# Kernel tuning notes

Hardware: AMD Instinct MI355X
Metric: run time of the kernel (lower is better)

## Reference

```python
import jax, jax.numpy as jnp
import numpy as np

B, M, FIN, K, FOUT, NNZ = 8, 40000, 64, 6, 64, 320000

def setup_inputs() -> dict:
    key = jax.random.key(0)
    k1, k2, k3, k4, k5 = jax.random.split(key, 5)
    x = jax.random.normal(k1, (B, M, FIN), dtype=jnp.float32)
    edge_rows = jax.random.randint(k2, (NNZ,), 0, M)
    edge_cols = jax.random.randint(k3, (NNZ,), 0, M)
    edge_vals = jax.random.normal(k4, (NNZ,), dtype=jnp.float32) * 0.1
    W = jax.random.normal(k5, (FIN * K, FOUT), dtype=jnp.float32) * 0.05
    return {"x": x, "edge_vals": edge_vals, "W": W,
            "edge_rows": edge_rows, "edge_cols": edge_cols}

def reference(x, edge_vals, W, edge_rows, edge_cols):
    Bd, Md, Fin = x.shape
    nK = W.shape[0] // Fin
    Fout = W.shape[1]
    # x0: [M, Fin*B] as in tf.transpose([1,2,0]) + reshape
    x0 = jnp.transpose(x, (1, 2, 0)).reshape(Md, Fin * Bd)

    def spmm_rescaled(v):
        # rescale_L(L, lmax=2) = L - I, so (L - I) @ v = L@v - v
        Lv = jax.ops.segment_sum(edge_vals[:, None] * v[edge_cols],
                                 edge_rows, num_segments=Md)
        return Lv - v

    xs = [x0]
    if nK > 1:
        x1 = spmm_rescaled(x0)
        xs.append(x1)
        xp, xc = x0, x1
        for _ in range(2, nK):
            xn = 2.0 * spmm_rescaled(xc) - xp  # Chebyshev recurrence
            xs.append(xn)
            xp, xc = xc, xn
    X = jnp.stack(xs, axis=0)                     # [K, M, Fin*B]
    X = X.reshape(nK, Md, Fin, Bd)                # split Fin*B -> (Fin, B)
    X = jnp.transpose(X, (3, 1, 2, 0))            # [B, M, Fin, K]
    X = X.reshape(Bd * Md, Fin * nK)
    out = (X @ W).reshape(Bd, Md, Fout)           # dense projection
    return out
```

## Files before the change

### kernel.cpp

```cpp
#include <hip/hip_runtime.h>

#define Mn    40000
#define Bn    8
#define FINn  64
#define Kn    6
#define FOUTn 64
#define NNZn  320000
#define Cn    512
#define NB    ((Mn + 255) / 256)
#define MT    (Mn / 64)


typedef _Float16 half8 __attribute__((ext_vector_type(8)));
typedef __attribute__((ext_vector_type(4))) float floatx4;

__device__ __forceinline__ ushort f2h(float f) {
    _Float16 h = (_Float16)f;
    return *(ushort*)&h;
}


__global__ __launch_bounds__(256) void k_hist(const int* __restrict__ rows,
                                              int* __restrict__ cnt) {
    int e = blockIdx.x * 256 + threadIdx.x;
    if (e < NNZn) atomicAdd(&cnt[rows[e]], 1);
}

__global__ __launch_bounds__(256) void k_scan_part(const int* __restrict__ cnt,
                                                   int* __restrict__ rowptr,
                                                   int* __restrict__ bsum) {
    __shared__ int part[256];
    int tid = threadIdx.x;
    int r = blockIdx.x * 256 + tid;
    int v = (r < Mn) ? cnt[r] : 0;
    part[tid] = v;
    __syncthreads();
    for (int off = 1; off < 256; off <<= 1) {
        int t = (tid >= off) ? part[tid - off] : 0;
        __syncthreads();
        part[tid] += t;
        __syncthreads();
    }
    if (r < Mn) rowptr[r] = part[tid] - v;
    if (tid == 255) bsum[blockIdx.x] = part[255];
}

__global__ __launch_bounds__(256) void k_scan_bsums(const int* __restrict__ bsum,
                                                    int* __restrict__ boff,
                                                    int* __restrict__ rowptr) {
    __shared__ int part[256];
    int tid = threadIdx.x;
    int v = (tid < NB) ? bsum[tid] : 0;
    part[tid] = v;
    __syncthreads();
    for (int off = 1; off < 256; off <<= 1) {
        int t = (tid >= off) ? part[tid - off] : 0;
        __syncthreads();
        part[tid] += t;
        __syncthreads();
    }
    if (tid < NB) boff[tid] = part[tid] - v;
    if (tid == 255) rowptr[Mn] = part[255];
}

__global__ __launch_bounds__(256) void k_scan_add(int* __restrict__ rowptr,
                                                  const int* __restrict__ boff,
                                                  int* __restrict__ wcur) {
    int r = blockIdx.x * 256 + threadIdx.x;
    if (r < Mn) {
        int v = rowptr[r] + boff[blockIdx.x];
        rowptr[r] = v;
        wcur[r] = v;
    }
}

__global__ __launch_bounds__(256) void k_scatter(const int* __restrict__ rows,
                                                 const int* __restrict__ cols,
                                                 const float* __restrict__ vals,
                                                 int* __restrict__ wcur,
                                                 int2* __restrict__ csr) {
    int e = blockIdx.x * 256 + threadIdx.x;
    if (e < NNZn) {
        int p = atomicAdd(&wcur[rows[e]], 1);
        int2 cv; cv.x = cols[e]; cv.y = __float_as_int(vals[e]);
        csr[p] = cv;
    }
}


__global__ __launch_bounds__(256) void k_transpose_h(const float* __restrict__ x,
                                                     ushort* __restrict__ x0h) {
    int m0 = blockIdx.x * 4;
    int t  = threadIdx.x;
#pragma unroll
    for (int k = 0; k < 2; ++k) {
        int i   = t + k * 256;
        int ml  = i >> 7;
        int rem = i & 127;
        int b   = rem >> 4;
        int fq  = (rem & 15) * 4;
        float4 a = *(const float4*)(x + ((size_t)b * Mn + m0 + ml) * 64 + fq);
        union { uint2 u; ushort h[4]; } s;
        s.h[0] = f2h(a.x); s.h[1] = f2h(a.y); s.h[2] = f2h(a.z); s.h[3] = f2h(a.w);
        *(uint2*)(x0h + (size_t)(m0 + ml) * Cn + b * 64 + fq) = s.u;
    }
}


__device__ __forceinline__ void fmah8(float* a, uint4 g, float w) {
    union { uint4 u; _Float16 h[8]; } c; c.u = g;
#pragma unroll
    for (int i = 0; i < 8; ++i) a[i] += w * (float)c.h[i];
}

__global__ __launch_bounds__(256) void k_spmm_h(const ushort* __restrict__ xc,
                                                const ushort* __restrict__ xp,
                                                ushort* __restrict__ xn,
                                                const int* __restrict__ rowptr,
                                                const int2* __restrict__ csr,
                                                int first) {
    int t = threadIdx.x;
    int lane = t & 63;
    int m = blockIdx.x * 4 + (t >> 6);
    const uint4* xc4 = (const uint4*)xc;
    uint4 v = xc4[(size_t)m * 64 + lane];
    uint4 p;
    if (!first) p = ((const uint4*)xp)[(size_t)m * 64 + lane];
    float a[8];
    { union { uint4 u; _Float16 h[8]; } c; c.u = v;
#pragma unroll
      for (int i = 0; i < 8; ++i) a[i] = -(float)c.h[i]; }

    int e = rowptr[m], end = rowptr[m + 1];
    for (; e + 8 <= end; e += 8) {
        int2 cv[8];
#pragma unroll
        for (int i = 0; i < 8; ++i) cv[i] = csr[e + i];
        uint4 g[8];
#pragma unroll
        for (int i = 0; i < 8; ++i) g[i] = xc4[(size_t)cv[i].x * 64 + lane];
#pragma unroll
        for (int i = 0; i < 8; ++i) fmah8(a, g[i], __int_as_float(cv[i].y));
    }
    for (; e + 4 <= end; e += 4) {
        int2 cv0 = csr[e],     cv1 = csr[e + 1];
        int2 cv2 = csr[e + 2], cv3 = csr[e + 3];
        uint4 g0 = xc4[(size_t)cv0.x * 64 + lane];
        uint4 g1 = xc4[(size_t)cv1.x * 64 + lane];
        uint4 g2 = xc4[(size_t)cv2.x * 64 + lane];
        uint4 g3 = xc4[(size_t)cv3.x * 64 + lane];
        fmah8(a, g0, __int_as_float(cv0.y));
        fmah8(a, g1, __int_as_float(cv1.y));
        fmah8(a, g2, __int_as_float(cv2.y));
        fmah8(a, g3, __int_as_float(cv3.y));
    }
    for (; e < end; ++e) {
        int2 cv = csr[e];
        uint4 g = xc4[(size_t)cv.x * 64 + lane];
        fmah8(a, g, __int_as_float(cv.y));
    }

    if (!first) {
        union { uint4 u; _Float16 h[8]; } c; c.u = p;
#pragma unroll
        for (int i = 0; i < 8; ++i) a[i] = 2.f * a[i] - (float)c.h[i];
    }
    union { uint4 u; _Float16 h[8]; } s;
#pragma unroll
    for (int i = 0; i < 8; ++i) s.h[i] = (_Float16)a[i];
    ((uint4*)xn)[(size_t)m * 64 + lane] = s.u;
}


__global__ __launch_bounds__(256) void k_wfrag(const float* __restrict__ W,
                                               ushort* __restrict__ wfrag) {
    int idx = blockIdx.x * 256 + threadIdx.x;
    if (idx >= 12 * 4 * 64 * 8) return;
    int j    = idx & 7;
    int lane = (idx >> 3) & 63;
    int n    = (idx >> 9) & 3;
    int kk   = idx >> 11;
    int k    = (lane >> 4) * 8 + j;
    int lev  = kk >> 1;
    int f    = (kk & 1) * 32 + k;
    int fo   = n * 16 + (lane & 15);
    wfrag[idx] = f2h(W[(f * Kn + lev) * FOUTn + fo]);
}


__global__ __launch_bounds__(256, 2) void k_gemm_mfma(const ushort* __restrict__ xh,
                                                      const ushort* __restrict__ wfrag,
                                                      float* __restrict__ out) {
    int t     = threadIdx.x;
    int wv    = t >> 6;
    int lane  = t & 63;
    int q     = lane >> 4, r = lane & 15;
    int mtile = blockIdx.x % MT;
    int b     = blockIdx.x / MT;
    int m0    = mtile * 64;

    const size_t lstrideH = (size_t)Mn * Cn;
    const ushort* abase = xh + (size_t)(m0 + wv * 16 + r) * Cn + b * 64 + q * 8;

    half8 aA0 = *(const half8*)(abase);
    half8 aB0 = *(const half8*)(abase + 32);
    half8 aA1 = *(const half8*)(abase + 1 * lstrideH);
    half8 aB1 = *(const half8*)(abase + 1 * lstrideH + 32);
    half8 aA2 = *(const half8*)(abase + 2 * lstrideH);
    half8 aB2 = *(const half8*)(abase + 2 * lstrideH + 32);
    half8 aA3 = *(const half8*)(abase + 3 * lstrideH);
    half8 aB3 = *(const half8*)(abase + 3 * lstrideH + 32);
    half8 aA4 = *(const half8*)(abase + 4 * lstrideH);
    half8 aB4 = *(const half8*)(abase + 4 * lstrideH + 32);
    half8 aA5 = *(const half8*)(abase + 5 * lstrideH);
    half8 aB5 = *(const half8*)(abase + 5 * lstrideH + 32);
    __builtin_amdgcn_sched_barrier(0);

    floatx4 acc[4];
    acc[0] = (floatx4)0.f; acc[1] = (floatx4)0.f;
    acc[2] = (floatx4)0.f; acc[3] = (floatx4)0.f;

#define MC_HALF(kkg, af)                                                              \
    do {                                                                              \
        const ushort* wf = wfrag + ((size_t)((kkg) * 4) * 64 + lane) * 8;             \
        acc[0] = __builtin_amdgcn_mfma_f32_16x16x32_f16(af, *(const half8*)(wf),        acc[0], 0, 0, 0); \
        acc[1] = __builtin_amdgcn_mfma_f32_16x16x32_f16(af, *(const half8*)(wf + 512),  acc[1], 0, 0, 0); \
        acc[2] = __builtin_amdgcn_mfma_f32_16x16x32_f16(af, *(const half8*)(wf + 1024), acc[2], 0, 0, 0); \
        acc[3] = __builtin_amdgcn_mfma_f32_16x16x32_f16(af, *(const half8*)(wf + 1536), acc[3], 0, 0, 0); \
    } while (0)

    MC_HALF(0,  aA0); MC_HALF(1,  aB0);
    MC_HALF(2,  aA1); MC_HALF(3,  aB1);
    MC_HALF(4,  aA2); MC_HALF(5,  aB2);
    MC_HALF(6,  aA3); MC_HALF(7,  aB3);
    MC_HALF(8,  aA4); MC_HALF(9,  aB4);
    MC_HALF(10, aA5); MC_HALF(11, aB5);
#undef MC_HALF

    size_t obase = ((size_t)b * Mn + m0 + wv * 16) * FOUTn;
#pragma unroll
    for (int n = 0; n < 4; ++n) {
#pragma unroll
        for (int reg = 0; reg < 4; ++reg) {
            int orow = q * 4 + reg;
            out[obase + (size_t)orow * FOUTn + n * 16 + r] = acc[n][reg];
        }
    }
}


__global__ __launch_bounds__(512) void k_transpose_f(const float* __restrict__ x,
                                                     float* __restrict__ x0) {
    int m = blockIdx.x, t = threadIdx.x;
    int b = t >> 6, f = t & 63;
    x0[(size_t)m * Cn + t] = x[((size_t)b * Mn + m) * 64 + f];
}

__global__ __launch_bounds__(256) void k_spmm_f32(const float4* __restrict__ xc,
                                                  const float4* __restrict__ xp,
                                                  float4* __restrict__ xn,
                                                  const int* __restrict__ rowptr,
                                                  const int2* __restrict__ csr,
                                                  int first) {
    int t = threadIdx.x;
    int lane = t & 63;
    int m = blockIdx.x * 4 + (t >> 6);
    size_t rb = (size_t)m * 128;
    float4 v0 = xc[rb + lane];
    float4 v1 = xc[rb + 64 + lane];
    float4 a0 = make_float4(-v0.x, -v0.y, -v0.z, -v0.w);
    float4 a1 = make_float4(-v1.x, -v1.y, -v1.z, -v1.w);
    int e = rowptr[m], end = rowptr[m + 1];
    for (; e < end; ++e) {
        int2 cv = csr[e];
        float w = __int_as_float(cv.y);
        const float4* r = xc + (size_t)cv.x * 128;
        float4 g0 = r[lane], g1 = r[64 + lane];
        a0.x += w * g0.x; a0.y += w * g0.y; a0.z += w * g0.z; a0.w += w * g0.w;
        a1.x += w * g1.x; a1.y += w * g1.y; a1.z += w * g1.z; a1.w += w * g1.w;
    }
    if (!first) {
        float4 p0 = xp[rb + lane];
        float4 p1 = xp[rb + 64 + lane];
        a0.x = 2.f * a0.x - p0.x; a0.y = 2.f * a0.y - p0.y;
        a0.z = 2.f * a0.z - p0.z; a0.w = 2.f * a0.w - p0.w;
        a1.x = 2.f * a1.x - p1.x; a1.y = 2.f * a1.y - p1.y;
        a1.z = 2.f * a1.z - p1.z; a1.w = 2.f * a1.w - p1.w;
    }
    xn[rb + lane] = a0;
    xn[rb + 64 + lane] = a1;
}

__global__ __launch_bounds__(256) void k_gemm2(const float* __restrict__ xa,
                                               const float* __restrict__ xb,
                                               const float* __restrict__ W,
                                               float* __restrict__ out,
                                               int ka, int kb, int accum) {
    __shared__ __align__(16) float Wa[64 * 64];
    __shared__ __align__(16) float Wb[64 * 64];
    __shared__ __align__(16) float xsa[4 * Cn];
    __shared__ __align__(16) float xsb[4 * Cn];
    int t = threadIdx.x;
    size_t m0 = (size_t)blockIdx.x * 4;
    for (int i = t; i < 4096; i += 256) {
        int f = i >> 6, fo = i & 63;
        Wa[i] = W[(f * Kn + ka) * FOUTn + fo];
        Wb[i] = W[(f * Kn + kb) * FOUTn + fo];
    }
    for (int i = t; i < 4 * Cn; i += 256) {
        xsa[i] = xa[m0 * Cn + i];
        xsb[i] = xb[m0 * Cn + i];
    }
    __syncthreads();
    int fo  = (t & 15) * 4;
    int idx = t >> 4;
    int m   = idx & 3;
    int bq  = idx >> 2;
    float4 acc0 = make_float4(0.f, 0.f, 0.f, 0.f);
    float4 acc1 = make_float4(0.f, 0.f, 0.f, 0.f);
    for (int f = 0; f < 64; ++f) {
        float4 wa = *(const float4*)&Wa[f * 64 + fo];
        float a0 = xsa[m * Cn + bq * 64 + f];
        float a1 = xsa[m * Cn + (bq + 4) * 64 + f];
        acc0.x += a0 * wa.x; acc0.y += a0 * wa.y; acc0.z += a0 * wa.z; acc0.w += a0 * wa.w;
        acc1.x += a1 * wa.x; acc1.y += a1 * wa.y; acc1.z += a1 * wa.z; acc1.w += a1 * wa.w;
        float4 wb = *(const float4*)&Wb[f * 64 + fo];
        float b0 = xsb[m * Cn + bq * 64 + f];
        float b1 = xsb[m * Cn + (bq + 4) * 64 + f];
        acc0.x += b0 * wb.x; acc0.y += b0 * wb.y; acc0.z += b0 * wb.z; acc0.w += b0 * wb.w;
        acc1.x += b1 * wb.x; acc1.y += b1 * wb.y; acc1.z += b1 * wb.z; acc1.w += b1 * wb.w;
    }
    size_t o0 = (((size_t)bq * Mn) + (m0 + m)) * FOUTn + fo;
    size_t o1 = (((size_t)(bq + 4) * Mn) + (m0 + m)) * FOUTn + fo;
    float4* out4_0 = (float4*)&out[o0];
    float4* out4_1 = (float4*)&out[o1];
    if (accum) {
        float4 c0 = *out4_0, c1 = *out4_1;
        acc0.x += c0.x; acc0.y += c0.y; acc0.z += c0.z; acc0.w += c0.w;
        acc1.x += c1.x; acc1.y += c1.y; acc1.z += c1.z; acc1.w += c1.w;
    }
    *out4_0 = acc0;
    *out4_1 = acc1;
}


extern "C" void kernel_launch(void* const* d_in, const int* in_sizes, int n_in,
                              void* d_out, int out_size, void* d_ws, size_t ws_size,
                              hipStream_t stream) {
    const float* x         = (const float*)d_in[0];
    const float* edge_vals = (const float*)d_in[1];
    const float* W         = (const float*)d_in[2];
    const int*   edge_rows = (const int*)d_in[3];
    const int*   edge_cols = (const int*)d_in[4];
    float* out = (float*)d_out;

    char* ws = (char*)d_ws;
    const size_t bufB = (size_t)Mn * Cn * sizeof(float);
    const size_t bufH = (size_t)Mn * Cn * sizeof(ushort);
    const size_t wfB  = 12 * 4 * 64 * 8 * sizeof(ushort);
    const size_t csrB = (size_t)(Mn + 4 + Mn) * 4 + (size_t)NNZn * 8;

    const int spmm_grid = Mn / 4;
    const int gemm_grid = MT * 8;

    if (ws_size >= 6 * bufH + wfB + csrB) {
        ushort* xh  = (ushort*)ws;
        ushort* wfr = (ushort*)(ws + 6 * bufH);
        int*    rowptr = (int*)(ws + 6 * bufH + wfB);
        int*    fill   = rowptr + (Mn + 4);
        int2*   csr    = (int2*)(fill + Mn);
        int*    bsum   = (int*)csr;
        int*    boff   = bsum + 256;
        ushort* slot[6];
        for (int l = 0; l < 6; ++l) slot[l] = xh + (size_t)l * Mn * Cn;

        hipMemsetAsync(fill, 0, Mn * sizeof(int), stream);
        k_hist<<<(NNZn + 255) / 256, 256, 0, stream>>>(edge_rows, fill);
        k_scan_part<<<NB, 256, 0, stream>>>(fill, rowptr, bsum);
        k_scan_bsums<<<1, 256, 0, stream>>>(bsum, boff, rowptr);
        k_scan_add<<<NB, 256, 0, stream>>>(rowptr, boff, fill);
        k_scatter<<<(NNZn + 255) / 256, 256, 0, stream>>>(edge_rows, edge_cols,
                                                          edge_vals, fill, csr);
        k_wfrag<<<96, 256, 0, stream>>>(W, wfr);

        k_transpose_h<<<Mn / 4, 256, 0, stream>>>(x, slot[0]);
        k_spmm_h<<<spmm_grid, 256, 0, stream>>>(slot[0], slot[0], slot[1],
                                                rowptr, csr, 1);
        k_spmm_h<<<spmm_grid, 256, 0, stream>>>(slot[1], slot[0], slot[2],
                                                rowptr, csr, 0);
        k_spmm_h<<<spmm_grid, 256, 0, stream>>>(slot[2], slot[1], slot[3],
                                                rowptr, csr, 0);
        k_spmm_h<<<spmm_grid, 256, 0, stream>>>(slot[3], slot[2], slot[4],
                                                rowptr, csr, 0);
        k_spmm_h<<<spmm_grid, 256, 0, stream>>>(slot[4], slot[3], slot[5],
                                                rowptr, csr, 0);
        k_gemm_mfma<<<gemm_grid, 256, 0, stream>>>(xh, wfr, out);
    } else {
        float* buf0 = (float*)(ws);
        float* buf1 = (float*)(ws + bufB);
        float* buf2 = (float*)(ws + 2 * bufB);
        int*   rowptr = (int*)(ws + 3 * bufB);
        int*   fill   = rowptr + (Mn + 4);
        int2*  csr    = (int2*)(fill + Mn);
        int*   bsum   = (int*)csr;
        int*   boff   = bsum + 256;
        hipMemsetAsync(fill, 0, Mn * sizeof(int), stream);
        k_hist<<<(NNZn + 255) / 256, 256, 0, stream>>>(edge_rows, fill);
        k_scan_part<<<NB, 256, 0, stream>>>(fill, rowptr, bsum);
        k_scan_bsums<<<1, 256, 0, stream>>>(bsum, boff, rowptr);
        k_scan_add<<<NB, 256, 0, stream>>>(rowptr, boff, fill);
        k_scatter<<<(NNZn + 255) / 256, 256, 0, stream>>>(edge_rows, edge_cols,
                                                          edge_vals, fill, csr);
        k_transpose_f<<<Mn, 512, 0, stream>>>(x, buf0);
        k_spmm_f32<<<spmm_grid, 256, 0, stream>>>((const float4*)buf0, (const float4*)buf0,
                                                  (float4*)buf1, rowptr, csr, 1);
        k_gemm2<<<Mn / 4, 256, 0, stream>>>(buf0, buf1, W, out, 0, 1, 0);
        k_spmm_f32<<<spmm_grid, 256, 0, stream>>>((const float4*)buf1, (const float4*)buf0,
                                                  (float4*)buf2, rowptr, csr, 0);
        k_spmm_f32<<<spmm_grid, 256, 0, stream>>>((const float4*)buf2, (const float4*)buf1,
                                                  (float4*)buf0, rowptr, csr, 0);
        k_gemm2<<<Mn / 4, 256, 0, stream>>>(buf2, buf0, W, out, 2, 3, 1);
        k_spmm_f32<<<spmm_grid, 256, 0, stream>>>((const float4*)buf0, (const float4*)buf2,
                                                  (float4*)buf1, rowptr, csr, 0);
        k_spmm_f32<<<spmm_grid, 256, 0, stream>>>((const float4*)buf1, (const float4*)buf0,
                                                  (float4*)buf2, rowptr, csr, 0);
        k_gemm2<<<Mn / 4, 256, 0, stream>>>(buf1, buf2, W, out, 4, 5, 1);
    }
}
```

Before: 543.8 us.

## Column-block SpMM grid for cache locality and LDS-staged A tiles in MFMA GEMM

The half-precision SpMM now splits the 512 feature columns into 8 blocks of 64 and launches a separate grid slice per block. Each wave covers 8 rows by 8 lanes, so gathered neighbour rows touch a narrower column slice that is more likely to stay in cache. The edge loop becomes a wave-uniform loop over the longest row's degree with masked padding, which adds wasted iterations on uneven rows. The GEMM loads its A tiles into swizzled LDS via global_load_lds before the MFMAs, where before it used direct register loads; this adds LDS traffic and a barrier. The fp32 fallback path is left unchanged apart from its launch sizes.

New measurement: 552.6 us. About the same (+1.6%).

```diff
diff --git a/kernel.cpp b/kernel.cpp
--- a/kernel.cpp
+++ b/kernel.cpp
@@ -9,6 +9,8 @@
 #define Cn    512
 #define NB    ((Mn + 255) / 256)
 #define MT    (Mn / 64)
+#define NCB   8
+#define MCH   (Mn / 32)
 
 
 typedef _Float16 half8 __attribute__((ext_vector_type(8)));
@@ -17,6 +19,12 @@
 __device__ __forceinline__ ushort f2h(float f) {
     _Float16 h = (_Float16)f;
     return *(ushort*)&h;
+}
+
+__device__ __forceinline__ void gl_lds16(const ushort* g, ushort* l) {
+    __builtin_amdgcn_global_load_lds(
+        (const __attribute__((address_space(1))) unsigned int*)g,
+        (__attribute__((address_space(3))) unsigned int*)l, 16, 0, 0);
 }
 
 
@@ -119,45 +127,38 @@
                                                 const int* __restrict__ rowptr,
                                                 const int2* __restrict__ csr,
                                                 int first) {
-    int t = threadIdx.x;
+    int t    = threadIdx.x;
     int lane = t & 63;
-    int m = blockIdx.x * 4 + (t >> 6);
+    int wv   = t >> 6;
+    int cblk = blockIdx.x / MCH;
+    int mch  = blockIdx.x % MCH;
+    int r    = mch * 32 + wv * 8 + (lane >> 3);
+    int coff = cblk * 8 + (lane & 7);
+
     const uint4* xc4 = (const uint4*)xc;
-    uint4 v = xc4[(size_t)m * 64 + lane];
+    uint4 v = xc4[(size_t)r * 64 + coff];
     uint4 p;
-    if (!first) p = ((const uint4*)xp)[(size_t)m * 64 + lane];
+    if (!first) p = ((const uint4*)xp)[(size_t)r * 64 + coff];
+    int rp0 = rowptr[r], rp1 = rowptr[r + 1];
+
     float a[8];
     { union { uint4 u; _Float16 h[8]; } c; c.u = v;
 #pragma unroll
       for (int i = 0; i < 8; ++i) a[i] = -(float)c.h[i]; }
 
-    int e = rowptr[m], end = rowptr[m + 1];
-    for (; e + 8 <= end; e += 8) {
-        int2 cv[8];
-#pragma unroll
-        for (int i = 0; i < 8; ++i) cv[i] = csr[e + i];
-        uint4 g[8];
-#pragma unroll
-        for (int i = 0; i < 8; ++i) g[i] = xc4[(size_t)cv[i].x * 64 + lane];
-#pragma unroll
-        for (int i = 0; i < 8; ++i) fmah8(a, g[i], __int_as_float(cv[i].y));
-    }
-    for (; e + 4 <= end; e += 4) {
-        int2 cv0 = csr[e],     cv1 = csr[e + 1];
-        int2 cv2 = csr[e + 2], cv3 = csr[e + 3];
-        uint4 g0 = xc4[(size_t)cv0.x * 64 + lane];
-        uint4 g1 = xc4[(size_t)cv1.x * 64 + lane];
-        uint4 g2 = xc4[(size_t)cv2.x * 64 + lane];
-        uint4 g3 = xc4[(size_t)cv3.x * 64 + lane];
-        fmah8(a, g0, __int_as_float(cv0.y));
-        fmah8(a, g1, __int_as_float(cv1.y));
-        fmah8(a, g2, __int_as_float(cv2.y));
-        fmah8(a, g3, __int_as_float(cv3.y));
-    }
-    for (; e < end; ++e) {
-        int2 cv = csr[e];
-        uint4 g = xc4[(size_t)cv.x * 64 + lane];
-        fmah8(a, g, __int_as_float(cv.y));
+    int it = 0;
+    while (__any(rp0 + it < rp1)) {
+#pragma unroll
+        for (int u = 0; u < 4; ++u) {
+            int e  = rp0 + it + u;
+            int ec = (e < rp1) ? e : (rp1 - 1);
+            ec = (ec < 0) ? 0 : ec;
+            int2 cv = csr[ec];
+            float w = (e < rp1) ? __int_as_float(cv.y) : 0.f;
+            uint4 g = xc4[(size_t)cv.x * 64 + coff];
+            fmah8(a, g, w);
+        }
+        it += 4;
     }
 
     if (!first) {
@@ -168,7 +169,7 @@
     union { uint4 u; _Float16 h[8]; } s;
 #pragma unroll
     for (int i = 0; i < 8; ++i) s.h[i] = (_Float16)a[i];
-    ((uint4*)xn)[(size_t)m * 64 + lane] = s.u;
+    ((uint4*)xn)[(size_t)r * 64 + coff] = s.u;
 }
 
 
@@ -191,6 +192,7 @@
 __global__ __launch_bounds__(256, 2) void k_gemm_mfma(const ushort* __restrict__ xh,
                                                       const ushort* __restrict__ wfrag,
                                                       float* __restrict__ out) {
+    __shared__ __align__(16) ushort As[6][64 * 64];
     int t     = threadIdx.x;
     int wv    = t >> 6;
     int lane  = t & 63;
@@ -200,41 +202,40 @@
     int m0    = mtile * 64;
 
     const size_t lstrideH = (size_t)Mn * Cn;
-    const ushort* abase = xh + (size_t)(m0 + wv * 16 + r) * Cn + b * 64 + q * 8;
-
-    half8 aA0 = *(const half8*)(abase);
-    half8 aB0 = *(const half8*)(abase + 32);
-    half8 aA1 = *(const half8*)(abase + 1 * lstrideH);
-    half8 aB1 = *(const half8*)(abase + 1 * lstrideH + 32);
-    half8 aA2 = *(const half8*)(abase + 2 * lstrideH);
-    half8 aB2 = *(const half8*)(abase + 2 * lstrideH + 32);
-    half8 aA3 = *(const half8*)(abase + 3 * lstrideH);
-    half8 aB3 = *(const half8*)(abase + 3 * lstrideH + 32);
-    half8 aA4 = *(const half8*)(abase + 4 * lstrideH);
-    half8 aB4 = *(const half8*)(abase + 4 * lstrideH + 32);
-    half8 aA5 = *(const half8*)(abase + 5 * lstrideH);
-    half8 aB5 = *(const half8*)(abase + 5 * lstrideH + 32);
-    __builtin_amdgcn_sched_barrier(0);
+
+    int srow = wv * 8 + (lane >> 3);
+    int gsw  = (lane & 7) ^ (srow & 7);
+    const ushort* gs0 = xh + (size_t)(m0 + srow) * Cn + b * 64 + gsw * 8;
+    const ushort* gs1 = gs0 + (size_t)32 * Cn;
+#pragma unroll
+    for (int lev = 0; lev < 6; ++lev) {
+        gl_lds16(gs0 + lev * lstrideH, &As[lev][wv * 512]);
+        gl_lds16(gs1 + lev * lstrideH, &As[lev][2048 + wv * 512]);
+    }
+    __syncthreads();
 
     floatx4 acc[4];
     acc[0] = (floatx4)0.f; acc[1] = (floatx4)0.f;
     acc[2] = (floatx4)0.f; acc[3] = (floatx4)0.f;
 
-#define MC_HALF(kkg, af)                                                              \
+    int row = wv * 16 + r;
+#define MC_HALF(lev, half)                                                            \
     do {                                                                              \
-        const ushort* wf = wfrag + ((size_t)((kkg) * 4) * 64 + lane) * 8;             \
+        int gran = ((half) * 4 + q) ^ (row & 7);                                      \
+        half8 af = *(const half8*)&As[lev][row * 64 + (gran << 3)];                   \
+        const ushort* wf = wfrag + ((size_t)(((lev) * 2 + (half)) * 4) * 64 + lane) * 8; \
         acc[0] = __builtin_amdgcn_mfma_f32_16x16x32_f16(af, *(const half8*)(wf),        acc[0], 0, 0, 0); \
         acc[1] = __builtin_amdgcn_mfma_f32_16x16x32_f16(af, *(const half8*)(wf + 512),  acc[1], 0, 0, 0); \
         acc[2] = __builtin_amdgcn_mfma_f32_16x16x32_f16(af, *(const half8*)(wf + 1024), acc[2], 0, 0, 0); \
         acc[3] = __builtin_amdgcn_mfma_f32_16x16x32_f16(af, *(const half8*)(wf + 1536), acc[3], 0, 0, 0); \
     } while (0)
 
-    MC_HALF(0,  aA0); MC_HALF(1,  aB0);
-    MC_HALF(2,  aA1); MC_HALF(3,  aB1);
-    MC_HALF(4,  aA2); MC_HALF(5,  aB2);
-    MC_HALF(6,  aA3); MC_HALF(7,  aB3);
-    MC_HALF(8,  aA4); MC_HALF(9,  aB4);
-    MC_HALF(10, aA5); MC_HALF(11, aB5);
+    MC_HALF(0, 0); MC_HALF(0, 1);
+    MC_HALF(1, 0); MC_HALF(1, 1);
+    MC_HALF(2, 0); MC_HALF(2, 1);
+    MC_HALF(3, 0); MC_HALF(3, 1);
+    MC_HALF(4, 0); MC_HALF(4, 1);
+    MC_HALF(5, 0); MC_HALF(5, 1);
 #undef MC_HALF
 
     size_t obase = ((size_t)b * Mn + m0 + wv * 16) * FOUTn;
@@ -360,7 +361,7 @@
     const size_t wfB  = 12 * 4 * 64 * 8 * sizeof(ushort);
     const size_t csrB = (size_t)(Mn + 4 + Mn) * 4 + (size_t)NNZn * 8;
 
-    const int spmm_grid = Mn / 4;
+    const int spmm_grid = NCB * MCH;
     const int gemm_grid = MT * 8;
 
     if (ws_size >= 6 * bufH + wfB + csrB) {
@@ -412,18 +413,18 @@
         k_scatter<<<(NNZn + 255) / 256, 256, 0, stream>>>(edge_rows, edge_cols,
                                                           edge_vals, fill, csr);
         k_transpose_f<<<Mn, 512, 0, stream>>>(x, buf0);
-        k_spmm_f32<<<spmm_grid, 256, 0, stream>>>((const float4*)buf0, (const float4*)buf0,
-                                                  (float4*)buf1, rowptr, csr, 1);
+        k_spmm_f32<<<Mn / 4, 256, 0, stream>>>((const float4*)buf0, (const float4*)buf0,
+                                               (float4*)buf1, rowptr, csr, 1);
         k_gemm2<<<Mn / 4, 256, 0, stream>>>(buf0, buf1, W, out, 0, 1, 0);
-        k_spmm_f32<<<spmm_grid, 256, 0, stream>>>((const float4*)buf1, (const float4*)buf0,
-                                                  (float4*)buf2, rowptr, csr, 0);
-        k_spmm_f32<<<spmm_grid, 256, 0, stream>>>((const float4*)buf2, (const float4*)buf1,
-                                                  (float4*)buf0, rowptr, csr, 0);
+        k_spmm_f32<<<Mn / 4, 256, 0, stream>>>((const float4*)buf1, (const float4*)buf0,
+                                               (float4*)buf2, rowptr, csr, 0);
+        k_spmm_f32<<<Mn / 4, 256, 0, stream>>>((const float4*)buf2, (const float4*)buf1,
+                                               (float4*)buf0, rowptr, csr, 0);
         k_gemm2<<<Mn / 4, 256, 0, stream>>>(buf2, buf0, W, out, 2, 3, 1);
-        k_spmm_f32<<<spmm_grid, 256, 0, stream>>>((const float4*)buf0, (const float4*)buf2,
-                                                  (float4*)buf1, rowptr, csr, 0);
-        k_spmm_f32<<<spmm_grid, 256, 0, stream>>>((const float4*)buf1, (const float4*)buf0,
-                                                  (float4*)buf2, rowptr, csr, 0);
+        k_spmm_f32<<<Mn / 4, 256, 0, stream>>>((const float4*)buf0, (const float4*)buf2,
+                                               (float4*)buf1, rowptr, csr, 0);
+        k_spmm_f32<<<Mn / 4, 256, 0, stream>>>((const float4*)buf1, (const float4*)buf0,
+                                               (float4*)buf2, rowptr, csr, 0);
         k_gemm2<<<Mn / 4, 256, 0, stream>>>(buf1, buf2, W, out, 4, 5, 1);
     }
 }
```

## Stage GEMM A-tiles through LDS with double-buffered async loads

Applied to the files above, without the earlier changes.

The MFMA projection kernel no longer loads all six Chebyshev levels into registers up front. It now streams each level into a double-buffered, XOR-swizzled LDS tile using global_load_lds, with manual vmcnt waits, so loading level k+2 overlaps with the MFMAs for level k. Launch bounds rise to 4 waves per SIMD to allow higher occupancy. The fallback f32 path's spmm grid is also changed to Mn/4, which may be a different block count from before and does not run by default. The manual waitcnt handling relies on exact counts of outstanding loads, so any miscount would read stale LDS data.

Result: no change. 540.4 us (-0.6%).

```diff
diff --git a/kernel.cpp b/kernel.cpp
--- a/kernel.cpp
+++ b/kernel.cpp
@@ -17,6 +17,12 @@
 __device__ __forceinline__ ushort f2h(float f) {
     _Float16 h = (_Float16)f;
     return *(ushort*)&h;
+}
+
+__device__ __forceinline__ void gl_lds16(const ushort* g, ushort* l) {
+    __builtin_amdgcn_global_load_lds(
+        (const __attribute__((address_space(1))) unsigned int*)g,
+        (__attribute__((address_space(3))) unsigned int*)l, 16, 0, 0);
 }
 
 
@@ -188,9 +194,10 @@
 }
 
 
-__global__ __launch_bounds__(256, 2) void k_gemm_mfma(const ushort* __restrict__ xh,
+__global__ __launch_bounds__(256, 4) void k_gemm_mfma(const ushort* __restrict__ xh,
                                                       const ushort* __restrict__ wfrag,
                                                       float* __restrict__ out) {
+    __shared__ __align__(16) ushort As[2][4][1024];
     int t     = threadIdx.x;
     int wv    = t >> 6;
     int lane  = t & 63;
@@ -200,50 +207,62 @@
     int m0    = mtile * 64;
 
     const size_t lstrideH = (size_t)Mn * Cn;
-    const ushort* abase = xh + (size_t)(m0 + wv * 16 + r) * Cn + b * 64 + q * 8;
-
-    half8 aA0 = *(const half8*)(abase);
-    half8 aB0 = *(const half8*)(abase + 32);
-    half8 aA1 = *(const half8*)(abase + 1 * lstrideH);
-    half8 aB1 = *(const half8*)(abase + 1 * lstrideH + 32);
-    half8 aA2 = *(const half8*)(abase + 2 * lstrideH);
-    half8 aB2 = *(const half8*)(abase + 2 * lstrideH + 32);
-    half8 aA3 = *(const half8*)(abase + 3 * lstrideH);
-    half8 aB3 = *(const half8*)(abase + 3 * lstrideH + 32);
-    half8 aA4 = *(const half8*)(abase + 4 * lstrideH);
-    half8 aB4 = *(const half8*)(abase + 4 * lstrideH + 32);
-    half8 aA5 = *(const half8*)(abase + 5 * lstrideH);
-    half8 aB5 = *(const half8*)(abase + 5 * lstrideH + 32);
-    __builtin_amdgcn_sched_barrier(0);
-
-    floatx4 acc[4];
-    acc[0] = (floatx4)0.f; acc[1] = (floatx4)0.f;
-    acc[2] = (floatx4)0.f; acc[3] = (floatx4)0.f;
-
-#define MC_HALF(kkg, af)                                                              \
-    do {                                                                              \
+
+    int srow = lane >> 3;
+    int gsw  = (lane & 7) ^ (srow & 7);
+    const ushort* gsA = xh + (size_t)(m0 + wv * 16 + srow) * Cn + b * 64 + gsw * 8;
+    const ushort* gsB = gsA + 8 * (size_t)Cn;
+    int swz = r & 7;
+
+    floatx4 acc0 = (floatx4)0.f, acc1 = (floatx4)0.f;
+    floatx4 acc2 = (floatx4)0.f, acc3 = (floatx4)0.f;
+
+#define STAGE(lev, buf) do {                                       \
+        gl_lds16(gsA + (size_t)(lev) * lstrideH, &As[buf][wv][0]);   \
+        gl_lds16(gsB + (size_t)(lev) * lstrideH, &As[buf][wv][512]); \
+    } while (0)
+
+#define MC(kkg, af) do {                                                              \
         const ushort* wf = wfrag + ((size_t)((kkg) * 4) * 64 + lane) * 8;             \
-        acc[0] = __builtin_amdgcn_mfma_f32_16x16x32_f16(af, *(const half8*)(wf),        acc[0], 0, 0, 0); \
-        acc[1] = __builtin_amdgcn_mfma_f32_16x16x32_f16(af, *(const half8*)(wf + 512),  acc[1], 0, 0, 0); \
-        acc[2] = __builtin_amdgcn_mfma_f32_16x16x32_f16(af, *(const half8*)(wf + 1024), acc[2], 0, 0, 0); \
-        acc[3] = __builtin_amdgcn_mfma_f32_16x16x32_f16(af, *(const half8*)(wf + 1536), acc[3], 0, 0, 0); \
+        acc0 = __builtin_amdgcn_mfma_f32_16x16x32_f16(af, *(const half8*)(wf),        acc0, 0, 0, 0); \
+        acc1 = __builtin_amdgcn_mfma_f32_16x16x32_f16(af, *(const half8*)(wf + 512),  acc1, 0, 0, 0); \
+        acc2 = __builtin_amdgcn_mfma_f32_16x16x32_f16(af, *(const half8*)(wf + 1024), acc2, 0, 0, 0); \
+        acc3 = __builtin_amdgcn_mfma_f32_16x16x32_f16(af, *(const half8*)(wf + 1536), acc3, 0, 0, 0); \
     } while (0)
 
-    MC_HALF(0,  aA0); MC_HALF(1,  aB0);
-    MC_HALF(2,  aA1); MC_HALF(3,  aB1);
-    MC_HALF(4,  aA2); MC_HALF(5,  aB2);
-    MC_HALF(6,  aA3); MC_HALF(7,  aB3);
-    MC_HALF(8,  aA4); MC_HALF(9,  aB4);
-    MC_HALF(10, aA5); MC_HALF(11, aB5);
-#undef MC_HALF
+#define LEVEL(lev, buf, VMSTR) do {                                                   \
+        asm volatile("s_waitcnt vmcnt(" VMSTR ")" ::: "memory");                      \
+        __builtin_amdgcn_sched_barrier(0);                                            \
+        half8 af0 = *(const half8*)&As[buf][wv][r * 64 + (((0 + q) ^ swz) << 3)];     \
+        half8 af1 = *(const half8*)&As[buf][wv][r * 64 + (((4 + q) ^ swz) << 3)];     \
+        asm volatile("s_waitcnt lgkmcnt(0)" ::: "memory");                            \
+        __builtin_amdgcn_sched_barrier(0);                                            \
+        if ((lev) < 4) STAGE((lev) + 2, buf);                                         \
+        MC((lev) * 2, af0);                                                           \
+        MC((lev) * 2 + 1, af1);                                                       \
+    } while (0)
+
+    STAGE(0, 0);
+    STAGE(1, 1);
+    LEVEL(0, 0, "2");
+    LEVEL(1, 1, "2");
+    LEVEL(2, 0, "2");
+    LEVEL(3, 1, "2");
+    LEVEL(4, 0, "2");
+    LEVEL(5, 1, "0");
+
+#undef LEVEL
+#undef MC
+#undef STAGE
 
     size_t obase = ((size_t)b * Mn + m0 + wv * 16) * FOUTn;
 #pragma unroll
     for (int n = 0; n < 4; ++n) {
+        floatx4 av = (n == 0) ? acc0 : (n == 1) ? acc1 : (n == 2) ? acc2 : acc3;
 #pragma unroll
         for (int reg = 0; reg < 4; ++reg) {
             int orow = q * 4 + reg;
-            out[obase + (size_t)orow * FOUTn + n * 16 + r] = acc[n][reg];
+            out[obase + (size_t)orow * FOUTn + n * 16 + r] = av[reg];
         }
     }
 }
@@ -412,18 +431,18 @@
         k_scatter<<<(NNZn + 255) / 256, 256, 0, stream>>>(edge_rows, edge_cols,
                                                           edge_vals, fill, csr);
         k_transpose_f<<<Mn, 512, 0, stream>>>(x, buf0);
-        k_spmm_f32<<<spmm_grid, 256, 0, stream>>>((const float4*)buf0, (const float4*)buf0,
-                                                  (float4*)buf1, rowptr, csr, 1);
+        k_spmm_f32<<<Mn / 4, 256, 0, stream>>>((const float4*)buf0, (const float4*)buf0,
+                                               (float4*)buf1, rowptr, csr, 1);
         k_gemm2<<<Mn / 4, 256, 0, stream>>>(buf0, buf1, W, out, 0, 1, 0);
-        k_spmm_f32<<<spmm_grid, 256, 0, stream>>>((const float4*)buf1, (const float4*)buf0,
-                                                  (float4*)buf2, rowptr, csr, 0);
-        k_spmm_f32<<<spmm_grid, 256, 0, stream>>>((const float4*)buf2, (const float4*)buf1,
-                                                  (float4*)buf0, rowptr, csr, 0);
+        k_spmm_f32<<<Mn / 4, 256, 0, stream>>>((const float4*)buf1, (const float4*)buf0,
+                                               (float4*)buf2, rowptr, csr, 0);
+        k_spmm_f32<<<Mn / 4, 256, 0, stream>>>((const float4*)buf2, (const float4*)buf1,
+                                               (float4*)buf0, rowptr, csr, 0);
         k_gemm2<<<Mn / 4, 256, 0, stream>>>(buf2, buf0, W, out, 2, 3, 1);
-        k_spmm_f32<<<spmm_grid, 256, 0, stream>>>((const float4*)buf0, (const float4*)buf2,
-                                                  (float4*)buf1, rowptr, csr, 0);
-        k_spmm_f32<<<spmm_grid, 256, 0, stream>>>((const float4*)buf1, (const float4*)buf0,
-                                                  (float4*)buf2, rowptr, csr, 0);
+        k_spmm_f32<<<Mn / 4, 256, 0, stream>>>((const float4*)buf0, (const float4*)buf2,
+                                               (float4*)buf1, rowptr, csr, 0);
+        k_spmm_f32<<<Mn / 4, 256, 0, stream>>>((const float4*)buf1, (const float4*)buf0,
+                                               (float4*)buf2, rowptr, csr, 0);
         k_gemm2<<<Mn / 4, 256, 0, stream>>>(buf1, buf2, W, out, 4, 5, 1);
     }
 }
```
